# Kernel optimization log

Hardware: AMD Instinct MI355X
Metric: run time of the kernel (lower is better)

## Reference

```python
import jax, jax.numpy as jnp
import numpy as np

N_NODES = 100000
N_EDGES = 1600000
IN_CH = 128
OUT_CH = 64
HID = 2 * OUT_CH  # 128


def setup_inputs() -> dict:
    key = jax.random.key(0)
    ks = jax.random.split(key, 8)
    s = lambda fan_in: 1.0 / np.sqrt(fan_in)
    return {
        "x": jax.random.normal(ks[0], (N_NODES, IN_CH), jnp.float32),
        "edge_index": jax.random.randint(ks[1], (2, N_EDGES), 0, N_NODES, dtype=jnp.int32),
        "W1": jax.random.normal(ks[2], (IN_CH, HID), jnp.float32) * s(IN_CH),
        "b1": jnp.zeros((HID,), jnp.float32),
        "W2": jax.random.normal(ks[3], (HID, HID), jnp.float32) * s(HID),
        "b2": jnp.zeros((HID,), jnp.float32),
        "W3": jax.random.normal(ks[4], (HID, OUT_CH), jnp.float32) * s(HID),
        "b3": jnp.zeros((OUT_CH,), jnp.float32),
    }


def reference(x, edge_index, W1, b1, W2, b2, W3, b3):
    N = x.shape[0]
    # GCNConv (PyG semantics): add self-loops, symmetric deg^{-1/2} normalization,
    # linear transform, scatter-add aggregation at destination, then bias.
    loops = jnp.arange(N, dtype=edge_index.dtype)
    src = jnp.concatenate([edge_index[0], loops])  # [E+N]
    dst = jnp.concatenate([edge_index[1], loops])  # [E+N]
    deg = jnp.zeros((N,), x.dtype).at[dst].add(1.0)  # in-degree incl. self-loop
    dinv = jnp.where(deg > 0, jax.lax.rsqrt(deg), 0.0)
    norm = (dinv[src] * dinv[dst])[:, None]  # [E+N, 1]

    def gcn_conv(h, W, b):
        h = h @ W  # transform first (smaller when out < in)
        msg = h[src] * norm  # gather + normalize, [E+N, C]
        agg = jnp.zeros((N, h.shape[1]), h.dtype).at[dst].add(msg)  # scatter-add
        return agg + b

    h = jax.nn.relu(gcn_conv(x, W1, b1))
    h = jax.nn.relu(gcn_conv(h, W2, b2))
    h = gcn_conv(h, W3, b3)
    return jnp.min(h, axis=0)  # min-pool over nodes -> [OUT_CH]
```

## Files before the change

kernel.cpp:

```cpp
#include <hip/hip_runtime.h>
#include <stdint.h>
#include <stddef.h>
#include <float.h>

typedef short bf16x8 __attribute__((ext_vector_type(8)));
typedef float f32x4 __attribute__((ext_vector_type(4)));

static __device__ __forceinline__ unsigned enc_min(float v) {
  unsigned u = __float_as_uint(v);
  return (u & 0x80000000u) ? ~u : (u | 0x80000000u);
}
static __device__ __forceinline__ unsigned short f2bf(float f) {
  unsigned u = __float_as_uint(f);
  u += 0x7fffu + ((u >> 16) & 1u);
  return (unsigned short)(u >> 16);
}
static __device__ __forceinline__ float bf2f(unsigned short b) {
  return __uint_as_float(((unsigned)b) << 16);
}
static __device__ __forceinline__ void acc8w(float* a, uint4 v, float w) {
  a[0] = fmaf(w, __uint_as_float(v.x << 16), a[0]);
  a[1] = fmaf(w, __uint_as_float(v.x & 0xffff0000u), a[1]);
  a[2] = fmaf(w, __uint_as_float(v.y << 16), a[2]);
  a[3] = fmaf(w, __uint_as_float(v.y & 0xffff0000u), a[3]);
  a[4] = fmaf(w, __uint_as_float(v.z << 16), a[4]);
  a[5] = fmaf(w, __uint_as_float(v.z & 0xffff0000u), a[5]);
  a[6] = fmaf(w, __uint_as_float(v.w << 16), a[6]);
  a[7] = fmaf(w, __uint_as_float(v.w & 0xffff0000u), a[7]);
}

__global__ void k_prepw(const float* __restrict__ W1, const float* __restrict__ W2,
                        const float* __restrict__ W3,
                        unsigned short* __restrict__ w1h, unsigned short* __restrict__ w1l,
                        unsigned short* __restrict__ w2h, unsigned short* __restrict__ w2l,
                        unsigned short* __restrict__ w3h, unsigned short* __restrict__ w3l) {
  const int K = 128;
  int idx = blockIdx.x * 256 + threadIdx.x;
  const float* W;
  unsigned short *oh, *ol;
  int Nn, base;
  if (idx < 16384) { W = W1; Nn = 128; oh = w1h; ol = w1l; base = idx; }
  else if (idx < 32768) { W = W2; Nn = 128; oh = w2h; ol = w2l; base = idx - 16384; }
  else if (idx < 40960) { W = W3; Nn = 64; oh = w3h; ol = w3l; base = idx - 32768; }
  else return;
  int n = base / K, k = base % K;
  float w = W[(size_t)k * Nn + n];
  unsigned short h = f2bf(w);
  unsigned short l = f2bf(w - bf2f(h));
  int nf = n >> 4, mloc = n & 15, kci = k >> 5, quad = (k >> 3) & 3, j = k & 7;
  size_t o = ((size_t)((nf * 4 + kci) * 64 + quad * 16 + mloc)) * 8 + j;
  oh[o] = h;
  ol[o] = l;
}

template <int NFW>
static __device__ __forceinline__ void gemm_body(const float* __restrict__ A,
                                                 const unsigned short* __restrict__ Wfh,
                                                 const unsigned short* __restrict__ Wfl,
                                                 unsigned short* __restrict__ P, int M,
                                                 int blk) {
  const int K = 128;
  const int COUT = NFW * 64;
  __shared__ unsigned short Ah[64][136];
  __shared__ unsigned short Al[64][136];
  int tid = threadIdx.x;
  int m0 = blk * 64;
  int w = tid >> 6, lane = tid & 63;

  bf16x8 bh[NFW][4], bl[NFW][4];
#pragma unroll
  for (int i = 0; i < NFW; ++i)
#pragma unroll
    for (int kci = 0; kci < 4; ++kci) {
      size_t o = ((size_t)(((w * NFW + i) * 4 + kci) * 64 + lane)) * 8;
      bh[i][kci] = *(const bf16x8*)&Wfh[o];
      bl[i][kci] = *(const bf16x8*)&Wfl[o];
    }

#pragma unroll
  for (int q = 0; q < 8; ++q) {
    int f = q * 256 + tid;
    int m = f >> 5, k4 = f & 31;
    int row = m0 + m;
    if (row >= M) row = M - 1;
    float4 v = *(const float4*)&A[(size_t)row * K + k4 * 4];
    unsigned short h0 = f2bf(v.x), h1 = f2bf(v.y), h2 = f2bf(v.z), h3 = f2bf(v.w);
    unsigned short l0 = f2bf(v.x - bf2f(h0)), l1 = f2bf(v.y - bf2f(h1));
    unsigned short l2 = f2bf(v.z - bf2f(h2)), l3 = f2bf(v.w - bf2f(h3));
    uint2 hh, ll;
    hh.x = (unsigned)h0 | ((unsigned)h1 << 16);
    hh.y = (unsigned)h2 | ((unsigned)h3 << 16);
    ll.x = (unsigned)l0 | ((unsigned)l1 << 16);
    ll.y = (unsigned)l2 | ((unsigned)l3 << 16);
    *(uint2*)&Ah[m][k4 * 4] = hh;
    *(uint2*)&Al[m][k4 * 4] = ll;
  }
  __syncthreads();

  int mloc = lane & 15, quad = lane >> 4;
  f32x4 acc[4][NFW];
#pragma unroll
  for (int rt = 0; rt < 4; ++rt)
#pragma unroll
    for (int i = 0; i < NFW; ++i) acc[rt][i] = (f32x4){0.f, 0.f, 0.f, 0.f};

#pragma unroll
  for (int rt = 0; rt < 4; ++rt) {
    const unsigned short* ph = &Ah[rt * 16 + mloc][quad * 8];
    const unsigned short* pl = &Al[rt * 16 + mloc][quad * 8];
#pragma unroll
    for (int kci = 0; kci < 4; ++kci) {
      bf16x8 ah = *(const bf16x8*)(ph + kci * 32);
      bf16x8 al = *(const bf16x8*)(pl + kci * 32);
#pragma unroll
      for (int i = 0; i < NFW; ++i) {
        acc[rt][i] = __builtin_amdgcn_mfma_f32_16x16x32_bf16(al, bh[i][kci], acc[rt][i], 0, 0, 0);
        acc[rt][i] = __builtin_amdgcn_mfma_f32_16x16x32_bf16(ah, bl[i][kci], acc[rt][i], 0, 0, 0);
        acc[rt][i] = __builtin_amdgcn_mfma_f32_16x16x32_bf16(ah, bh[i][kci], acc[rt][i], 0, 0, 0);
      }
    }
  }

#pragma unroll
  for (int rt = 0; rt < 4; ++rt) {
    int rbase = m0 + rt * 16 + quad * 4;
#pragma unroll
    for (int r = 0; r < 4; ++r) {
      int row = rbase + r;
      if (row < M) {
#pragma unroll
        for (int i = 0; i < NFW; ++i) {
          int nf = w * NFW + i;
          P[(size_t)row * COUT + nf * 16 + mloc] = f2bf(acc[rt][i][r]);
        }
      }
    }
  }
}

__global__ __launch_bounds__(256) void k_count_gemm(const int* __restrict__ edge, int E, int N,
                                                    int* __restrict__ cnt8,
                                                    int* __restrict__ bin_cur,
                                                    int2* __restrict__ pairs,
                                                    int binw, int bcap,
                                                    const float* __restrict__ X,
                                                    const unsigned short* __restrict__ w1h,
                                                    const unsigned short* __restrict__ w1l,
                                                    unsigned short* __restrict__ P1,
                                                    int ncb) {
  if ((int)blockIdx.x >= ncb) {
    gemm_body<2>(X, w1h, w1l, P1, N, blockIdx.x - ncb);
    return;
  }
  __shared__ int h[8], gbase[8], lfill[8];
  int cslot = blockIdx.x & 7;
  int* cnt = cnt8 + (size_t)cslot * N;
  int tid = threadIdx.x;
  int nt = (E + 1023) >> 10;
  for (int t = blockIdx.x; t < nt; t += ncb) {
    int e0 = t << 10;
    if (tid < 8) { h[tid] = 0; lfill[tid] = 0; }
    __syncthreads();
    int d[4], s[4], g[4], r[4];
#pragma unroll
    for (int k = 0; k < 4; ++k) {
      int e = e0 + tid + k * 256;
      d[k] = -1;
      if (e < E) {
        d[k] = edge[E + e];
        s[k] = edge[e];
        g[k] = (int)((unsigned)d[k] / (unsigned)binw);
        r[k] = atomicAdd(&cnt[d[k]], 1);
        atomicAdd(&h[g[k]], 1);
      }
    }
    __syncthreads();
    if (tid < 8) gbase[tid] = atomicAdd(&bin_cur[tid], h[tid]);
    __syncthreads();
#pragma unroll
    for (int k = 0; k < 4; ++k) {
      if (d[k] >= 0) {
        int rr = atomicAdd(&lfill[g[k]], 1);
        int p = gbase[g[k]] + rr;
        unsigned packed = (unsigned)d[k] | ((unsigned)cslot << 17) | ((unsigned)r[k] << 20);
        if (p < bcap) pairs[(size_t)g[k] * bcap + p] = make_int2((int)packed, s[k]);
      }
    }
    __syncthreads();
  }
}

__global__ void k_scan1(const int* __restrict__ cnt8, int N,
                        int* __restrict__ cnt, int* __restrict__ incl,
                        int* __restrict__ bsum) {
  __shared__ int sm[1024];
  int tid = threadIdx.x;
  int i = blockIdx.x * 1024 + tid;
  int v = 0;
  if (i < N) {
#pragma unroll
    for (int g = 0; g < 8; ++g) v += cnt8[(size_t)g * N + i];
    cnt[i] = v;
  }
  sm[tid] = v;
  __syncthreads();
  for (int off = 1; off < 1024; off <<= 1) {
    int t = (tid >= off) ? sm[tid - off] : 0;
    __syncthreads();
    sm[tid] += t;
    __syncthreads();
  }
  if (i < N) incl[i] = sm[tid];
  if (tid == 1023) bsum[blockIdx.x] = sm[1023];
}

__global__ void k_scan2(const int* __restrict__ bsum, int nb, int* __restrict__ boff) {
  __shared__ int sm[128];
  int tid = threadIdx.x;
  int v = (tid < nb) ? bsum[tid] : 0;
  sm[tid] = v;
  __syncthreads();
  for (int off = 1; off < 128; off <<= 1) {
    int t = (tid >= off) ? sm[tid - off] : 0;
    __syncthreads();
    sm[tid] += t;
    __syncthreads();
  }
  if (tid < nb) boff[tid] = sm[tid] - v;
}

__global__ void k_aux(const int* __restrict__ cnt, const int* __restrict__ cnt8,
                      const int* __restrict__ incl, const int* __restrict__ boff,
                      int N, int E, int* __restrict__ row_ptr,
                      int* __restrict__ base8, float* __restrict__ dinv) {
  int i = blockIdx.x * blockDim.x + threadIdx.x;
  if (i < N) {
    int rp = incl[i] - cnt[i] + boff[i >> 10];
    row_ptr[i] = rp;
    dinv[i] = 1.0f / sqrtf((float)(cnt[i] + 1));
    int run = rp;
#pragma unroll
    for (int c = 0; c < 8; ++c) {
      base8[(size_t)c * N + i] = run;
      run += cnt8[(size_t)c * N + i];
    }
  } else if (i == N) {
    row_ptr[N] = E;
  }
}

__global__ __launch_bounds__(256) void k_scatter(const int2* __restrict__ pairs,
                                                 const int* __restrict__ bin_cur, int bcap,
                                                 const int* __restrict__ base8, int N,
                                                 int* __restrict__ srcs) {
  int grp = blockIdx.x & 7;
  int bslot = blockIdx.x >> 3;
  int nslot = gridDim.x >> 3;
  int cnt_g = bin_cur[grp];
  if (cnt_g > bcap) cnt_g = bcap;
  const int2* pp = pairs + (size_t)grp * bcap;
  for (int i = bslot * blockDim.x + threadIdx.x; i < cnt_g; i += nslot * blockDim.x) {
    int2 pr = pp[i];
    unsigned w = (unsigned)pr.x;
    int d = (int)(w & 0x1FFFFu);
    int c = (int)((w >> 17) & 7u);
    int r = (int)(w >> 20);
    srcs[base8[(size_t)c * N + d] + r] = pr.y;
  }
}

template <int NFW>
__global__ __launch_bounds__(256) void k_agg_gemm(const unsigned short* __restrict__ Pin,
                                                  const int* __restrict__ row_ptr,
                                                  const int* __restrict__ srcs,
                                                  const float* __restrict__ dinv,
                                                  const float* __restrict__ bias,
                                                  const unsigned short* __restrict__ Wfh,
                                                  const unsigned short* __restrict__ Wfl,
                                                  unsigned short* __restrict__ Pout, int N) {
  const int COUT = NFW * 64;
  __shared__ unsigned short Ah[16][136];
  __shared__ unsigned short Al[16][136];
  int tid = threadIdx.x;
  int wv = tid >> 6, lane = tid & 63;
  int grp = lane >> 4, sub = lane & 15;
  int m = wv * 4 + grp;
  int d = blockIdx.x * 16 + m;
  int dc = d < N ? d : N - 1;
  bool valid = d < N;
  unsigned soff = (unsigned)sub * 16u;
  const char* Pb = (const char*)Pin;

  float dv = dinv[dc];
  float a[8] = {0.f, 0.f, 0.f, 0.f, 0.f, 0.f, 0.f, 0.f};
  {
    uint4 v = *(const uint4*)(Pb + ((unsigned)dc * 256u + soff));
    acc8w(a, v, dv);
  }
  int lo = row_ptr[dc];
  int hi = row_ptr[valid ? d + 1 : dc];
  int j = lo;
  for (; j + 8 <= hi; j += 8) {
    unsigned id[8];
    float dw[8];
    uint4 vv[8];
#pragma unroll
    for (int k = 0; k < 8; ++k) id[k] = (unsigned)srcs[j + k];
#pragma unroll
    for (int k = 0; k < 8; ++k) dw[k] = dinv[id[k]];
#pragma unroll
    for (int k = 0; k < 8; ++k) vv[k] = *(const uint4*)(Pb + (id[k] * 256u + soff));
#pragma unroll
    for (int k = 0; k < 8; ++k) acc8w(a, vv[k], dw[k]);
  }
  for (; j + 4 <= hi; j += 4) {
    unsigned id[4];
    float dw[4];
    uint4 vv[4];
#pragma unroll
    for (int k = 0; k < 4; ++k) id[k] = (unsigned)srcs[j + k];
#pragma unroll
    for (int k = 0; k < 4; ++k) dw[k] = dinv[id[k]];
#pragma unroll
    for (int k = 0; k < 4; ++k) vv[k] = *(const uint4*)(Pb + (id[k] * 256u + soff));
#pragma unroll
    for (int k = 0; k < 4; ++k) acc8w(a, vv[k], dw[k]);
  }
  for (; j < hi; ++j) {
    unsigned i0 = (unsigned)srcs[j];
    float w0 = dinv[i0];
    uint4 v0 = *(const uint4*)(Pb + (i0 * 256u + soff));
    acc8w(a, v0, w0);
  }

  bf16x8 bh[NFW][4], bl[NFW][4];
#pragma unroll
  for (int i = 0; i < NFW; ++i)
#pragma unroll
    for (int kci = 0; kci < 4; ++kci) {
      size_t o = ((size_t)(((wv * NFW + i) * 4 + kci) * 64 + lane)) * 8;
      bh[i][kci] = *(const bf16x8*)&Wfh[o];
      bl[i][kci] = *(const bf16x8*)&Wfl[o];
    }

  int ch0 = sub * 8;
  float4 bv0 = *(const float4*)&bias[ch0];
  float4 bv1 = *(const float4*)&bias[ch0 + 4];
  float h[8];
  h[0] = dv * a[0] + bv0.x; h[1] = dv * a[1] + bv0.y;
  h[2] = dv * a[2] + bv0.z; h[3] = dv * a[3] + bv0.w;
  h[4] = dv * a[4] + bv1.x; h[5] = dv * a[5] + bv1.y;
  h[6] = dv * a[6] + bv1.z; h[7] = dv * a[7] + bv1.w;
#pragma unroll
  for (int k = 0; k < 8; ++k) h[k] = fmaxf(h[k], 0.f);
  unsigned short hb[8], lb[8];
#pragma unroll
  for (int k = 0; k < 8; ++k) {
    hb[k] = f2bf(h[k]);
    lb[k] = f2bf(h[k] - bf2f(hb[k]));
  }
  uint4 HH, LL;
  HH.x = (unsigned)hb[0] | ((unsigned)hb[1] << 16);
  HH.y = (unsigned)hb[2] | ((unsigned)hb[3] << 16);
  HH.z = (unsigned)hb[4] | ((unsigned)hb[5] << 16);
  HH.w = (unsigned)hb[6] | ((unsigned)hb[7] << 16);
  LL.x = (unsigned)lb[0] | ((unsigned)lb[1] << 16);
  LL.y = (unsigned)lb[2] | ((unsigned)lb[3] << 16);
  LL.z = (unsigned)lb[4] | ((unsigned)lb[5] << 16);
  LL.w = (unsigned)lb[6] | ((unsigned)lb[7] << 16);
  *(uint4*)&Ah[m][ch0] = HH;
  *(uint4*)&Al[m][ch0] = LL;
  __syncthreads();

  int mloc = lane & 15, quad = lane >> 4;
  f32x4 acc[NFW];
#pragma unroll
  for (int i = 0; i < NFW; ++i) acc[i] = (f32x4){0.f, 0.f, 0.f, 0.f};
#pragma unroll
  for (int kci = 0; kci < 4; ++kci) {
    bf16x8 ah = *(const bf16x8*)&Ah[mloc][quad * 8 + kci * 32];
    bf16x8 al = *(const bf16x8*)&Al[mloc][quad * 8 + kci * 32];
#pragma unroll
    for (int i = 0; i < NFW; ++i) {
      acc[i] = __builtin_amdgcn_mfma_f32_16x16x32_bf16(al, bh[i][kci], acc[i], 0, 0, 0);
      acc[i] = __builtin_amdgcn_mfma_f32_16x16x32_bf16(ah, bl[i][kci], acc[i], 0, 0, 0);
      acc[i] = __builtin_amdgcn_mfma_f32_16x16x32_bf16(ah, bh[i][kci], acc[i], 0, 0, 0);
    }
  }
  int rbase = blockIdx.x * 16 + quad * 4;
#pragma unroll
  for (int r = 0; r < 4; ++r) {
    int row = rbase + r;
    if (row < N) {
#pragma unroll
      for (int i = 0; i < NFW; ++i) {
        int nf = wv * NFW + i;
        Pout[(size_t)row * COUT + nf * 16 + mloc] = f2bf(acc[i][r]);
      }
    }
  }
}

__global__ __launch_bounds__(256) void k_agg_pool(const unsigned short* __restrict__ P,
                                                  const int* __restrict__ row_ptr,
                                                  const int* __restrict__ srcs,
                                                  const float* __restrict__ dinv,
                                                  const float* __restrict__ bias,
                                                  unsigned* __restrict__ minenc, int N) {
  __shared__ float s_red[4][64];
  int tid = threadIdx.x;
  int wv = tid >> 6, lane = tid & 63;
  int g = lane >> 3, q = lane & 7;
  int d = blockIdx.x * 32 + wv * 8 + g;
  bool valid = d < N;
  int dc = valid ? d : N - 1;
  const char* Pb = (const char*)P;
  unsigned soff = (unsigned)q * 16u;

  float dv = dinv[dc];
  float a[8] = {0.f, 0.f, 0.f, 0.f, 0.f, 0.f, 0.f, 0.f};
  {
    uint4 v = *(const uint4*)(Pb + ((unsigned)dc * 128u + soff));
    acc8w(a, v, dv);
  }
  int lo = row_ptr[dc];
  int hi = row_ptr[valid ? d + 1 : dc];
  int j = lo;
  for (; j + 8 <= hi; j += 8) {
    unsigned id[8];
    float dw[8];
    uint4 vv[8];
#pragma unroll
    for (int k = 0; k < 8; ++k) id[k] = (unsigned)srcs[j + k];
#pragma unroll
    for (int k = 0; k < 8; ++k) dw[k] = dinv[id[k]];
#pragma unroll
    for (int k = 0; k < 8; ++k) vv[k] = *(const uint4*)(Pb + (id[k] * 128u + soff));
#pragma unroll
    for (int k = 0; k < 8; ++k) acc8w(a, vv[k], dw[k]);
  }
  for (; j < hi; ++j) {
    unsigned i0 = (unsigned)srcs[j];
    float w0 = dinv[i0];
    uint4 v0 = *(const uint4*)(Pb + (i0 * 128u + soff));
    acc8w(a, v0, w0);
  }

  int c0 = q * 8;
  float4 bv0 = *(const float4*)&bias[c0];
  float4 bv1 = *(const float4*)&bias[c0 + 4];
  float h[8];
  h[0] = dv * a[0] + bv0.x; h[1] = dv * a[1] + bv0.y;
  h[2] = dv * a[2] + bv0.z; h[3] = dv * a[3] + bv0.w;
  h[4] = dv * a[4] + bv1.x; h[5] = dv * a[5] + bv1.y;
  h[6] = dv * a[6] + bv1.z; h[7] = dv * a[7] + bv1.w;
  if (!valid) {
#pragma unroll
    for (int k = 0; k < 8; ++k) h[k] = FLT_MAX;
  }
#pragma unroll
  for (int off = 8; off < 64; off <<= 1) {
#pragma unroll
    for (int k = 0; k < 8; ++k) h[k] = fminf(h[k], __shfl_xor(h[k], off, 64));
  }
  if (lane < 8) {
#pragma unroll
    for (int k = 0; k < 8; ++k) s_red[wv][q * 8 + k] = h[k];
  }
  __syncthreads();
  if (tid < 64) {
    float mn = fminf(fminf(s_red[0][tid], s_red[1][tid]),
                     fminf(s_red[2][tid], s_red[3][tid]));
    atomicMin(&minenc[tid], enc_min(mn));
  }
}

__global__ void k_decode(const unsigned* __restrict__ minenc, float* __restrict__ out) {
  int c = threadIdx.x;
  unsigned k = minenc[c];
  unsigned u = (k & 0x80000000u) ? (k & 0x7FFFFFFFu) : ~k;
  out[c] = __uint_as_float(u);
}

extern "C" void kernel_launch(void* const* d_in, const int* in_sizes, int n_in,
                              void* d_out, int out_size, void* d_ws, size_t ws_size,
                              hipStream_t stream) {
  const float* X  = (const float*)d_in[0];
  const int* edge = (const int*)d_in[1];
  const float* W1 = (const float*)d_in[2];
  const float* b1 = (const float*)d_in[3];
  const float* W2 = (const float*)d_in[4];
  const float* b2 = (const float*)d_in[5];
  const float* W3 = (const float*)d_in[6];
  const float* b3 = (const float*)d_in[7];
  float* out = (float*)d_out;

  const int IN_CH = 128;
  int N = in_sizes[0] / IN_CH;
  int E = in_sizes[1] / 2;

  char* ws = (char*)d_ws;
  size_t off = 0;
  auto alloc = [&](size_t bytes) {
    void* p = ws + off;
    off = (off + bytes + 255) & ~(size_t)255;
    return p;
  };
  unsigned short* P1 = (unsigned short*)alloc((size_t)N * 128 * 2);
  unsigned short* P2 = (unsigned short*)alloc((size_t)N * 128 * 2);
  int* srcs      = (int*)alloc((size_t)E * 4);
  int* cnt8      = (int*)alloc((size_t)8 * N * 4);
  int* base8     = (int*)alloc((size_t)8 * N * 4);
  int* cnt       = (int*)alloc((size_t)N * 4);
  int* incl      = (int*)alloc((size_t)N * 4);
  int* row_ptr   = (int*)alloc((size_t)(N + 1) * 4);
  float* dinv    = (float*)alloc((size_t)N * 4);
  int* bsum      = (int*)alloc(1024);
  int* boff      = (int*)alloc(1024);
  int* bin_cur   = (int*)alloc(256);
  unsigned* minenc = (unsigned*)alloc(256);
  unsigned short* w1h = (unsigned short*)alloc(16384 * 2);
  unsigned short* w1l = (unsigned short*)alloc(16384 * 2);
  unsigned short* w2h = (unsigned short*)alloc(16384 * 2);
  unsigned short* w2l = (unsigned short*)alloc(16384 * 2);
  unsigned short* w3h = (unsigned short*)alloc(8192 * 2);
  unsigned short* w3l = (unsigned short*)alloc(8192 * 2);

  int bcap = E / 8 + 65536;
  int binw = (N + 7) / 8;
  int2* pairs = (int2*)P2;
  unsigned short* P3 = P1;

  hipMemsetAsync(cnt8, 0, (size_t)8 * N * 4, stream);
  hipMemsetAsync(bin_cur, 0, 32, stream);
  hipMemsetAsync(minenc, 0xFF, 64 * 4, stream);

  int nb = (N + 1023) / 1024;
  int gx = (N + 63) / 64;
  int ncb = 782;
  int gagg = (N + 15) / 16;
  int gpool = (N + 31) / 32;
  k_prepw<<<160, 256, 0, stream>>>(W1, W2, W3, w1h, w1l, w2h, w2l, w3h, w3l);
  k_count_gemm<<<ncb + gx, 256, 0, stream>>>(edge, E, N, cnt8, bin_cur, pairs, binw, bcap,
                                             X, w1h, w1l, P1, ncb);
  k_scan1<<<nb, 1024, 0, stream>>>(cnt8, N, cnt, incl, bsum);
  k_scan2<<<1, 128, 0, stream>>>(bsum, nb, boff);
  k_aux<<<(N + 256) / 256, 256, 0, stream>>>(cnt, cnt8, incl, boff, N, E, row_ptr, base8, dinv);
  k_scatter<<<2048, 256, 0, stream>>>(pairs, bin_cur, bcap, base8, N, srcs);
  k_agg_gemm<2><<<gagg, 256, 0, stream>>>(P1, row_ptr, srcs, dinv, b1, w2h, w2l, P2, N);
  k_agg_gemm<1><<<gagg, 256, 0, stream>>>(P2, row_ptr, srcs, dinv, b2, w3h, w3l, P3, N);
  k_agg_pool<<<gpool, 256, 0, stream>>>(P3, row_ptr, srcs, dinv, b3, minenc, N);
  k_decode<<<1, 64, 0, stream>>>(minenc, out);
}
```

Measured before the change: 436.9 us.

## Prescale GEMM outputs by source dinv and fuse first GEMM with CSR scatter

The source-side deg^{-1/2} factor is folded into each GEMM epilogue, so the aggregation loops no longer gather dinv per edge and can use plain adds instead of weighted FMAs. This requires dinv before the first GEMM, so that GEMM moves out of the counting kernel and is co-launched with the CSR scatter kernel. It removes one random 4-byte gather per edge per layer, at the cost of the first GEMM no longer overlapping the edge-counting pass. The destination scaling is still applied after accumulation.

```diff
diff --git a/kernel.cpp b/kernel.cpp
--- a/kernel.cpp
+++ b/kernel.cpp
@@ -18,15 +18,117 @@
 static __device__ __forceinline__ float bf2f(unsigned short b) {
   return __uint_as_float(((unsigned)b) << 16);
 }
-static __device__ __forceinline__ void acc8w(float* a, uint4 v, float w) {
-  a[0] = fmaf(w, __uint_as_float(v.x << 16), a[0]);
-  a[1] = fmaf(w, __uint_as_float(v.x & 0xffff0000u), a[1]);
-  a[2] = fmaf(w, __uint_as_float(v.y << 16), a[2]);
-  a[3] = fmaf(w, __uint_as_float(v.y & 0xffff0000u), a[3]);
-  a[4] = fmaf(w, __uint_as_float(v.z << 16), a[4]);
-  a[5] = fmaf(w, __uint_as_float(v.z & 0xffff0000u), a[5]);
-  a[6] = fmaf(w, __uint_as_float(v.w << 16), a[6]);
-  a[7] = fmaf(w, __uint_as_float(v.w & 0xffff0000u), a[7]);
+static __device__ __forceinline__ void acc8(float* a, uint4 v) {
+  a[0] += __uint_as_float(v.x << 16);
+  a[1] += __uint_as_float(v.x & 0xffff0000u);
+  a[2] += __uint_as_float(v.y << 16);
+  a[3] += __uint_as_float(v.y & 0xffff0000u);
+  a[4] += __uint_as_float(v.z << 16);
+  a[5] += __uint_as_float(v.z & 0xffff0000u);
+  a[6] += __uint_as_float(v.w << 16);
+  a[7] += __uint_as_float(v.w & 0xffff0000u);
+}
+
+__global__ __launch_bounds__(256) void k_count_bin(const int* __restrict__ edge, int E, int N,
+                                                   int* __restrict__ cnt8,
+                                                   int* __restrict__ bin_cur,
+                                                   int2* __restrict__ pairs,
+                                                   int binw, int bcap) {
+  __shared__ int h[8], gbase[8], lfill[8];
+  int cslot = blockIdx.x & 7;
+  int* cnt = cnt8 + (size_t)cslot * N;
+  int tid = threadIdx.x;
+  int nt = (E + 1023) >> 10;
+  for (int t = blockIdx.x; t < nt; t += gridDim.x) {
+    int e0 = t << 10;
+    if (tid < 8) { h[tid] = 0; lfill[tid] = 0; }
+    __syncthreads();
+    int d[4], s[4], g[4], r[4];
+#pragma unroll
+    for (int k = 0; k < 4; ++k) {
+      int e = e0 + tid + k * 256;
+      d[k] = -1;
+      if (e < E) {
+        d[k] = edge[E + e];
+        s[k] = edge[e];
+        g[k] = (int)((unsigned)d[k] / (unsigned)binw);
+        r[k] = atomicAdd(&cnt[d[k]], 1);
+        atomicAdd(&h[g[k]], 1);
+      }
+    }
+    __syncthreads();
+    if (tid < 8) gbase[tid] = atomicAdd(&bin_cur[tid], h[tid]);
+    __syncthreads();
+#pragma unroll
+    for (int k = 0; k < 4; ++k) {
+      if (d[k] >= 0) {
+        int rr = atomicAdd(&lfill[g[k]], 1);
+        int p = gbase[g[k]] + rr;
+        unsigned packed = (unsigned)d[k] | ((unsigned)cslot << 17) | ((unsigned)r[k] << 20);
+        if (p < bcap) pairs[(size_t)g[k] * bcap + p] = make_int2((int)packed, s[k]);
+      }
+    }
+    __syncthreads();
+  }
+}
+
+__global__ void k_scan1(const int* __restrict__ cnt8, int N,
+                        int* __restrict__ cnt, int* __restrict__ incl,
+                        int* __restrict__ bsum) {
+  __shared__ int sm[1024];
+  int tid = threadIdx.x;
+  int i = blockIdx.x * 1024 + tid;
+  int v = 0;
+  if (i < N) {
+#pragma unroll
+    for (int g = 0; g < 8; ++g) v += cnt8[(size_t)g * N + i];
+    cnt[i] = v;
+  }
+  sm[tid] = v;
+  __syncthreads();
+  for (int off = 1; off < 1024; off <<= 1) {
+    int t = (tid >= off) ? sm[tid - off] : 0;
+    __syncthreads();
+    sm[tid] += t;
+    __syncthreads();
+  }
+  if (i < N) incl[i] = sm[tid];
+  if (tid == 1023) bsum[blockIdx.x] = sm[1023];
+}
+
+__global__ void k_scan2(const int* __restrict__ bsum, int nb, int* __restrict__ boff) {
+  __shared__ int sm[128];
+  int tid = threadIdx.x;
+  int v = (tid < nb) ? bsum[tid] : 0;
+  sm[tid] = v;
+  __syncthreads();
+  for (int off = 1; off < 128; off <<= 1) {
+    int t = (tid >= off) ? sm[tid - off] : 0;
+    __syncthreads();
+    sm[tid] += t;
+    __syncthreads();
+  }
+  if (tid < nb) boff[tid] = sm[tid] - v;
+}
+
+__global__ void k_aux(const int* __restrict__ cnt, const int* __restrict__ cnt8,
+                      const int* __restrict__ incl, const int* __restrict__ boff,
+                      int N, int E, int* __restrict__ row_ptr,
+                      int* __restrict__ base8, float* __restrict__ dinv) {
+  int i = blockIdx.x * blockDim.x + threadIdx.x;
+  if (i < N) {
+    int rp = incl[i] - cnt[i] + boff[i >> 10];
+    row_ptr[i] = rp;
+    dinv[i] = 1.0f / sqrtf((float)(cnt[i] + 1));
+    int run = rp;
+#pragma unroll
+    for (int c = 0; c < 8; ++c) {
+      base8[(size_t)c * N + i] = run;
+      run += cnt8[(size_t)c * N + i];
+    }
+  } else if (i == N) {
+    row_ptr[N] = E;
+  }
 }
 
 __global__ void k_prepw(const float* __restrict__ W1, const float* __restrict__ W2,
@@ -57,6 +159,7 @@
 static __device__ __forceinline__ void gemm_body(const float* __restrict__ A,
                                                  const unsigned short* __restrict__ Wfh,
                                                  const unsigned short* __restrict__ Wfl,
+                                                 const float* __restrict__ dinv,
                                                  unsigned short* __restrict__ P, int M,
                                                  int blk) {
   const int K = 128;
@@ -128,144 +231,43 @@
     for (int r = 0; r < 4; ++r) {
       int row = rbase + r;
       if (row < M) {
+        float dv = dinv[row];
 #pragma unroll
         for (int i = 0; i < NFW; ++i) {
           int nf = w * NFW + i;
-          P[(size_t)row * COUT + nf * 16 + mloc] = f2bf(acc[rt][i][r]);
+          P[(size_t)row * COUT + nf * 16 + mloc] = f2bf(acc[rt][i][r] * dv);
         }
       }
     }
   }
 }
 
-__global__ __launch_bounds__(256) void k_count_gemm(const int* __restrict__ edge, int E, int N,
-                                                    int* __restrict__ cnt8,
-                                                    int* __restrict__ bin_cur,
-                                                    int2* __restrict__ pairs,
-                                                    int binw, int bcap,
-                                                    const float* __restrict__ X,
-                                                    const unsigned short* __restrict__ w1h,
-                                                    const unsigned short* __restrict__ w1l,
-                                                    unsigned short* __restrict__ P1,
-                                                    int ncb) {
-  if ((int)blockIdx.x >= ncb) {
-    gemm_body<2>(X, w1h, w1l, P1, N, blockIdx.x - ncb);
-    return;
-  }
-  __shared__ int h[8], gbase[8], lfill[8];
-  int cslot = blockIdx.x & 7;
-  int* cnt = cnt8 + (size_t)cslot * N;
-  int tid = threadIdx.x;
-  int nt = (E + 1023) >> 10;
-  for (int t = blockIdx.x; t < nt; t += ncb) {
-    int e0 = t << 10;
-    if (tid < 8) { h[tid] = 0; lfill[tid] = 0; }
-    __syncthreads();
-    int d[4], s[4], g[4], r[4];
-#pragma unroll
-    for (int k = 0; k < 4; ++k) {
-      int e = e0 + tid + k * 256;
-      d[k] = -1;
-      if (e < E) {
-        d[k] = edge[E + e];
-        s[k] = edge[e];
-        g[k] = (int)((unsigned)d[k] / (unsigned)binw);
-        r[k] = atomicAdd(&cnt[d[k]], 1);
-        atomicAdd(&h[g[k]], 1);
-      }
-    }
-    __syncthreads();
-    if (tid < 8) gbase[tid] = atomicAdd(&bin_cur[tid], h[tid]);
-    __syncthreads();
-#pragma unroll
-    for (int k = 0; k < 4; ++k) {
-      if (d[k] >= 0) {
-        int rr = atomicAdd(&lfill[g[k]], 1);
-        int p = gbase[g[k]] + rr;
-        unsigned packed = (unsigned)d[k] | ((unsigned)cslot << 17) | ((unsigned)r[k] << 20);
-        if (p < bcap) pairs[(size_t)g[k] * bcap + p] = make_int2((int)packed, s[k]);
-      }
-    }
-    __syncthreads();
-  }
-}
-
-__global__ void k_scan1(const int* __restrict__ cnt8, int N,
-                        int* __restrict__ cnt, int* __restrict__ incl,
-                        int* __restrict__ bsum) {
-  __shared__ int sm[1024];
-  int tid = threadIdx.x;
-  int i = blockIdx.x * 1024 + tid;
-  int v = 0;
-  if (i < N) {
-#pragma unroll
-    for (int g = 0; g < 8; ++g) v += cnt8[(size_t)g * N + i];
-    cnt[i] = v;
-  }
-  sm[tid] = v;
-  __syncthreads();
-  for (int off = 1; off < 1024; off <<= 1) {
-    int t = (tid >= off) ? sm[tid - off] : 0;
-    __syncthreads();
-    sm[tid] += t;
-    __syncthreads();
-  }
-  if (i < N) incl[i] = sm[tid];
-  if (tid == 1023) bsum[blockIdx.x] = sm[1023];
-}
-
-__global__ void k_scan2(const int* __restrict__ bsum, int nb, int* __restrict__ boff) {
-  __shared__ int sm[128];
-  int tid = threadIdx.x;
-  int v = (tid < nb) ? bsum[tid] : 0;
-  sm[tid] = v;
-  __syncthreads();
-  for (int off = 1; off < 128; off <<= 1) {
-    int t = (tid >= off) ? sm[tid - off] : 0;
-    __syncthreads();
-    sm[tid] += t;
-    __syncthreads();
-  }
-  if (tid < nb) boff[tid] = sm[tid] - v;
-}
-
-__global__ void k_aux(const int* __restrict__ cnt, const int* __restrict__ cnt8,
-                      const int* __restrict__ incl, const int* __restrict__ boff,
-                      int N, int E, int* __restrict__ row_ptr,
-                      int* __restrict__ base8, float* __restrict__ dinv) {
-  int i = blockIdx.x * blockDim.x + threadIdx.x;
-  if (i < N) {
-    int rp = incl[i] - cnt[i] + boff[i >> 10];
-    row_ptr[i] = rp;
-    dinv[i] = 1.0f / sqrtf((float)(cnt[i] + 1));
-    int run = rp;
-#pragma unroll
-    for (int c = 0; c < 8; ++c) {
-      base8[(size_t)c * N + i] = run;
-      run += cnt8[(size_t)c * N + i];
-    }
-  } else if (i == N) {
-    row_ptr[N] = E;
-  }
-}
-
-__global__ __launch_bounds__(256) void k_scatter(const int2* __restrict__ pairs,
-                                                 const int* __restrict__ bin_cur, int bcap,
-                                                 const int* __restrict__ base8, int N,
-                                                 int* __restrict__ srcs) {
-  int grp = blockIdx.x & 7;
-  int bslot = blockIdx.x >> 3;
-  int nslot = gridDim.x >> 3;
-  int cnt_g = bin_cur[grp];
-  if (cnt_g > bcap) cnt_g = bcap;
-  const int2* pp = pairs + (size_t)grp * bcap;
-  for (int i = bslot * blockDim.x + threadIdx.x; i < cnt_g; i += nslot * blockDim.x) {
-    int2 pr = pp[i];
-    unsigned w = (unsigned)pr.x;
-    int d = (int)(w & 0x1FFFFu);
-    int c = (int)((w >> 17) & 7u);
-    int r = (int)(w >> 20);
-    srcs[base8[(size_t)c * N + d] + r] = pr.y;
+__global__ __launch_bounds__(256) void k_fill_gemm(const float* __restrict__ A,
+                                                   const unsigned short* __restrict__ Wfh,
+                                                   const unsigned short* __restrict__ Wfl,
+                                                   const float* __restrict__ dinv,
+                                                   unsigned short* __restrict__ P, int M,
+                                                   const int2* __restrict__ pairs,
+                                                   const int* __restrict__ bin_cur, int bcap,
+                                                   const int* __restrict__ base8, int N,
+                                                   int* __restrict__ srcs, int ns) {
+  if ((int)blockIdx.x >= ns) {
+    gemm_body<2>(A, Wfh, Wfl, dinv, P, M, blockIdx.x - ns);
+  } else {
+    int grp = blockIdx.x & 7;
+    int bslot = blockIdx.x >> 3;
+    int nslot = ns >> 3;
+    int cnt_g = bin_cur[grp];
+    if (cnt_g > bcap) cnt_g = bcap;
+    const int2* pp = pairs + (size_t)grp * bcap;
+    for (int i = bslot * blockDim.x + threadIdx.x; i < cnt_g; i += nslot * blockDim.x) {
+      int2 pr = pp[i];
+      unsigned w = (unsigned)pr.x;
+      int d = (int)(w & 0x1FFFFu);
+      int c = (int)((w >> 17) & 7u);
+      int r = (int)(w >> 20);
+      srcs[base8[(size_t)c * N + d] + r] = pr.y;
+    }
   }
 }
 
@@ -291,46 +293,38 @@
   unsigned soff = (unsigned)sub * 16u;
   const char* Pb = (const char*)Pin;
 
-  float dv = dinv[dc];
   float a[8] = {0.f, 0.f, 0.f, 0.f, 0.f, 0.f, 0.f, 0.f};
   {
     uint4 v = *(const uint4*)(Pb + ((unsigned)dc * 256u + soff));
-    acc8w(a, v, dv);
+    acc8(a, v);
   }
   int lo = row_ptr[dc];
   int hi = row_ptr[valid ? d + 1 : dc];
   int j = lo;
   for (; j + 8 <= hi; j += 8) {
     unsigned id[8];
-    float dw[8];
     uint4 vv[8];
 #pragma unroll
     for (int k = 0; k < 8; ++k) id[k] = (unsigned)srcs[j + k];
 #pragma unroll
-    for (int k = 0; k < 8; ++k) dw[k] = dinv[id[k]];
-#pragma unroll
     for (int k = 0; k < 8; ++k) vv[k] = *(const uint4*)(Pb + (id[k] * 256u + soff));
 #pragma unroll
-    for (int k = 0; k < 8; ++k) acc8w(a, vv[k], dw[k]);
+    for (int k = 0; k < 8; ++k) acc8(a, vv[k]);
   }
   for (; j + 4 <= hi; j += 4) {
     unsigned id[4];
-    float dw[4];
     uint4 vv[4];
 #pragma unroll
     for (int k = 0; k < 4; ++k) id[k] = (unsigned)srcs[j + k];
 #pragma unroll
-    for (int k = 0; k < 4; ++k) dw[k] = dinv[id[k]];
-#pragma unroll
     for (int k = 0; k < 4; ++k) vv[k] = *(const uint4*)(Pb + (id[k] * 256u + soff));
 #pragma unroll
-    for (int k = 0; k < 4; ++k) acc8w(a, vv[k], dw[k]);
+    for (int k = 0; k < 4; ++k) acc8(a, vv[k]);
   }
   for (; j < hi; ++j) {
     unsigned i0 = (unsigned)srcs[j];
-    float w0 = dinv[i0];
     uint4 v0 = *(const uint4*)(Pb + (i0 * 256u + soff));
-    acc8w(a, v0, w0);
+    acc8(a, v0);
   }
 
   bf16x8 bh[NFW][4], bl[NFW][4];
@@ -343,6 +337,7 @@
       bl[i][kci] = *(const bf16x8*)&Wfl[o];
     }
 
+  float dv = dinv[dc];
   int ch0 = sub * 8;
   float4 bv0 = *(const float4*)&bias[ch0];
   float4 bv1 = *(const float4*)&bias[ch0 + 4];
@@ -392,10 +387,11 @@
   for (int r = 0; r < 4; ++r) {
     int row = rbase + r;
     if (row < N) {
+      float dvr = dinv[row];
 #pragma unroll
       for (int i = 0; i < NFW; ++i) {
         int nf = wv * NFW + i;
-        Pout[(size_t)row * COUT + nf * 16 + mloc] = f2bf(acc[i][r]);
+        Pout[(size_t)row * COUT + nf * 16 + mloc] = f2bf(acc[i][r] * dvr);
       }
     }
   }
@@ -417,35 +413,31 @@
   const char* Pb = (const char*)P;
   unsigned soff = (unsigned)q * 16u;
 
-  float dv = dinv[dc];
   float a[8] = {0.f, 0.f, 0.f, 0.f, 0.f, 0.f, 0.f, 0.f};
   {
     uint4 v = *(const uint4*)(Pb + ((unsigned)dc * 128u + soff));
-    acc8w(a, v, dv);
+    acc8(a, v);
   }
   int lo = row_ptr[dc];
   int hi = row_ptr[valid ? d + 1 : dc];
   int j = lo;
   for (; j + 8 <= hi; j += 8) {
     unsigned id[8];
-    float dw[8];
     uint4 vv[8];
 #pragma unroll
     for (int k = 0; k < 8; ++k) id[k] = (unsigned)srcs[j + k];
 #pragma unroll
-    for (int k = 0; k < 8; ++k) dw[k] = dinv[id[k]];
-#pragma unroll
     for (int k = 0; k < 8; ++k) vv[k] = *(const uint4*)(Pb + (id[k] * 128u + soff));
 #pragma unroll
-    for (int k = 0; k < 8; ++k) acc8w(a, vv[k], dw[k]);
+    for (int k = 0; k < 8; ++k) acc8(a, vv[k]);
   }
   for (; j < hi; ++j) {
     unsigned i0 = (unsigned)srcs[j];
-    float w0 = dinv[i0];
     uint4 v0 = *(const uint4*)(Pb + (i0 * 128u + soff));
-    acc8w(a, v0, w0);
-  }
-
+    acc8(a, v0);
+  }
+
+  float dv = dinv[dc];
   int c0 = q * 8;
   float4 bv0 = *(const float4*)&bias[c0];
   float4 bv1 = *(const float4*)&bias[c0 + 4];
@@ -537,16 +529,17 @@
 
   int nb = (N + 1023) / 1024;
   int gx = (N + 63) / 64;
-  int ncb = 782;
+  int ns = 1024;
   int gagg = (N + 15) / 16;
   int gpool = (N + 31) / 32;
   k_prepw<<<160, 256, 0, stream>>>(W1, W2, W3, w1h, w1l, w2h, w2l, w3h, w3l);
-  k_count_gemm<<<ncb + gx, 256, 0, stream>>>(edge, E, N, cnt8, bin_cur, pairs, binw, bcap,
-                                             X, w1h, w1l, P1, ncb);
+  k_count_bin<<<782, 256, 0, stream>>>(edge, E, N, cnt8, bin_cur, pairs, binw, bcap);
   k_scan1<<<nb, 1024, 0, stream>>>(cnt8, N, cnt, incl, bsum);
   k_scan2<<<1, 128, 0, stream>>>(bsum, nb, boff);
   k_aux<<<(N + 256) / 256, 256, 0, stream>>>(cnt, cnt8, incl, boff, N, E, row_ptr, base8, dinv);
-  k_scatter<<<2048, 256, 0, stream>>>(pairs, bin_cur, bcap, base8, N, srcs);
+
+  k_fill_gemm<<<ns + gx, 256, 0, stream>>>(X, w1h, w1l, dinv, P1, N,
+                                           pairs, bin_cur, bcap, base8, N, srcs, ns);
   k_agg_gemm<2><<<gagg, 256, 0, stream>>>(P1, row_ptr, srcs, dinv, b1, w2h, w2l, P2, N);
   k_agg_gemm<1><<<gagg, 256, 0, stream>>>(P2, row_ptr, srcs, dinv, b2, w3h, w3l, P3, N);
   k_agg_pool<<<gpool, 256, 0, stream>>>(P3, row_ptr, srcs, dinv, b3, minenc, N);
```

New measurement: 435.9 us. No clear change (-0.2%).
